# Kernel tuning notes

Hardware: AMD Instinct MI355X
Metric: run time of the kernel (lower is better)

Reference implementation:

```python
import jax, jax.numpy as jnp
import numpy as np

R = 512      # latent dim
M = 4        # center dimensionality
L = 256      # number of cluster centers
B = 8192     # batch
SIGMA_EPS = 1e-4


def setup_inputs() -> dict:
    key = jax.random.key(0)
    kx, kc = jax.random.split(key)
    x = jax.random.normal(kx, (B, R), dtype=jnp.float32)
    c = jax.random.normal(kc, (M, L), dtype=jnp.float32)   # codebook centers
    sigma = jnp.full((1,), 5.0, dtype=jnp.float32)         # trainable temperature
    return {"x": x, "c": c, "sigma": sigma}


def reference(x, c, sigma):
    b = x.shape[0]
    nf = R // M
    z = x.reshape(b, nf, M)                                # (b, nf, m)
    sig = jax.nn.relu(sigma[0]) + SIGMA_EPS
    # squared distances ||z - c||^2 over m, expanded to avoid (b,nf,m,L) materialization
    z_sq = jnp.sum(z * z, axis=-1, keepdims=True)          # (b, nf, 1)
    c_sq = jnp.sum(c * c, axis=0)                          # (L,)
    zc = jnp.einsum('bnm,ml->bnl', z, c)                   # (b, nf, L)
    dist = z_sq - 2.0 * zc + c_sq[None, None, :]           # (b, nf, L)
    q = jax.nn.softmax(-sig * dist, axis=-1)               # soft assignments (b, nf, L)
    out = jnp.einsum('bnl,ml->bnm', q, c)                  # weighted centers (b, nf, m)
    return out.reshape(b, R)
```

## Files before the change

### kernel.cpp

```cpp
#include <hip/hip_runtime.h>
#include <math.h>

#define RDIM 512
#define MDIM 4
#define LDIM 256
#define BDIM 8192
#define NROWS (BDIM * (RDIM / MDIM))
#define SIGMA_EPS 1e-4f
#define LOG2E 1.4426950408889634f

typedef _Float16 half4_t __attribute__((ext_vector_type(4)));
typedef _Float16 half8_t __attribute__((ext_vector_type(8)));
typedef __fp16   fp16x2_t __attribute__((ext_vector_type(2)));
typedef float    float4_t __attribute__((ext_vector_type(4)));

#define NRT (NROWS / 16)
#define MAIN_BLOCKS 2048
#define WPB 4
#define NT (NRT / (MAIN_BLOCKS * WPB))

__global__ void prep_kernel(const float* __restrict__ c, const float* __restrict__ sigma,
                            _Float16* __restrict__ a1w, _Float16* __restrict__ a2w) {
  const int gid  = blockIdx.x * 256 + threadIdx.x;
  const int lane = gid & 63;
  const int q4   = lane >> 4;
  const int m    = lane & 15;
  const float sig   = fmaxf(sigma[0], 0.0f) + SIGMA_EPS;
  const float sigL  = sig * LOG2E;
  const float sig2L = 2.0f * sigL;
  if (gid < 1024) {
    const int t = gid >> 6;
    const int l = t * 16 + m;
    float cv[4];
    cv[0] = c[l]; cv[1] = c[256 + l]; cv[2] = c[512 + l]; cv[3] = c[768 + l];
    _Float16 uh[4], ul[4];
    #pragma unroll
    for (int i = 0; i < 4; ++i) {
      float u = sig2L * cv[i];
      uh[i] = (_Float16)u;
      ul[i] = (_Float16)(u - (float)uh[i]);
    }
    float bias = -sigL * fmaf(cv[0], cv[0], fmaf(cv[1], cv[1], fmaf(cv[2], cv[2], cv[3] * cv[3])));
    _Float16 bh = (_Float16)bias;
    _Float16 bl = (_Float16)(bias - (float)bh);
    #pragma unroll
    for (int j = 0; j < 8; ++j) {
      int k = q4 * 8 + j;
      _Float16 v = (_Float16)0.0f;
      if      (k < 4)   v = uh[k];
      else if (k < 8)   v = uh[k - 4];
      else if (k < 12)  v = ul[k - 8];
      else if (k == 12) v = bh;
      else if (k == 13) v = bl;
      a1w[(t * 64 + lane) * 8 + j] = v;
    }
  } else if (gid < 1536) {
    const int p = (gid - 1024) >> 6;
    #pragma unroll
    for (int j = 0; j < 8; ++j) {
      int center = 32 * p + 16 * (j >> 2) + 4 * q4 + (j & 3);
      _Float16 v = (_Float16)0.0f;
      if (m < 4)       v = (_Float16)c[m * 256 + center];
      else if (m == 4) v = (_Float16)1.0f;
      a2w[(p * 64 + lane) * 8 + j] = v;
    }
  }
}

__global__ __launch_bounds__(256, 2) void sq_mfma_kernel(
    const float4* __restrict__ x4,
    const _Float16* __restrict__ a1w,
    const _Float16* __restrict__ a2w,
    float4* __restrict__ out4) {
  const int tid  = threadIdx.x;
  const int lane = tid & 63;
  const int wave = tid >> 6;
  const int q4   = lane >> 4;
  const int zr   = lane & 15;

  half8_t a1[16], a2[8];
  const half8_t* a1p = (const half8_t*)a1w;
  const half8_t* a2p = (const half8_t*)a2w;
  #pragma unroll
  for (int t = 0; t < 16; ++t) a1[t] = a1p[t * 64 + lane];
  #pragma unroll
  for (int p = 0; p < 8; ++p) a2[p] = a2p[p * 64 + lane];

  const int gw = blockIdx.x * WPB + wave;
  const float4_t zero4 = {0.f, 0.f, 0.f, 0.f};

  for (int it = 0; it < NT; ++it) {
    const int rowbase = (gw * NT + it) * 16;

    const float4 z = x4[rowbase + zr];
    _Float16 zh0 = (_Float16)z.x, zh1 = (_Float16)z.y, zh2 = (_Float16)z.z, zh3 = (_Float16)z.w;
    _Float16 zl0 = (_Float16)(z.x - (float)zh0);
    _Float16 zl1 = (_Float16)(z.y - (float)zh1);
    _Float16 zl2 = (_Float16)(z.z - (float)zh2);
    _Float16 zl3 = (_Float16)(z.w - (float)zh3);

    const _Float16 h0 = (_Float16)0.0f, h1 = (_Float16)1.0f;
    half8_t b1;
    b1[0] = (q4 < 2) ? zh0 : h0;
    b1[1] = (q4 < 2) ? zh1 : h0;
    b1[2] = (q4 < 2) ? zh2 : h0;
    b1[3] = (q4 < 2) ? zh3 : h0;
    b1[4] = (q4 == 0) ? zl0 : ((q4 == 1) ? h1 : h0);
    b1[5] = (q4 == 0) ? zl1 : ((q4 == 1) ? h1 : h0);
    b1[6] = (q4 == 0) ? zl2 : h0;
    b1[7] = (q4 == 0) ? zl3 : h0;

    float4_t s[16];
    #pragma unroll
    for (int t = 0; t < 16; ++t)
      s[t] = __builtin_amdgcn_mfma_f32_16x16x32_f16(a1[t], b1, zero4, 0, 0, 0);

    float mx = -3.0e38f;
    #pragma unroll
    for (int t = 0; t < 16; ++t)
      mx = fmaxf(mx, fmaxf(fmaxf(s[t][0], s[t][1]), fmaxf(s[t][2], s[t][3])));
    mx = fmaxf(mx, __shfl_xor(mx, 16));
    mx = fmaxf(mx, __shfl_xor(mx, 32));

    float4_t d2 = zero4;
    #pragma unroll
    for (int p = 0; p < 8; ++p) {
      fp16x2_t e01a = __builtin_amdgcn_cvt_pkrtz(
          __builtin_amdgcn_exp2f(s[2 * p][0] - mx), __builtin_amdgcn_exp2f(s[2 * p][1] - mx));
      fp16x2_t e23a = __builtin_amdgcn_cvt_pkrtz(
          __builtin_amdgcn_exp2f(s[2 * p][2] - mx), __builtin_amdgcn_exp2f(s[2 * p][3] - mx));
      fp16x2_t e01b = __builtin_amdgcn_cvt_pkrtz(
          __builtin_amdgcn_exp2f(s[2 * p + 1][0] - mx), __builtin_amdgcn_exp2f(s[2 * p + 1][1] - mx));
      fp16x2_t e23b = __builtin_amdgcn_cvt_pkrtz(
          __builtin_amdgcn_exp2f(s[2 * p + 1][2] - mx), __builtin_amdgcn_exp2f(s[2 * p + 1][3] - mx));
      half8_t b2;
      b2[0] = (_Float16)e01a[0]; b2[1] = (_Float16)e01a[1];
      b2[2] = (_Float16)e23a[0]; b2[3] = (_Float16)e23a[1];
      b2[4] = (_Float16)e01b[0]; b2[5] = (_Float16)e01b[1];
      b2[6] = (_Float16)e23b[0]; b2[7] = (_Float16)e23b[1];
      d2 = __builtin_amdgcn_mfma_f32_16x16x32_f16(a2[p], b2, d2, 0, 0, 0);
    }

    float den = __shfl(d2[0], zr + 16);
    if (lane < 16) {
      float r = __builtin_amdgcn_rcpf(den);
      float4 o = make_float4(d2[0] * r, d2[1] * r, d2[2] * r, d2[3] * r);
      out4[rowbase + zr] = o;
    }
  }
}

extern "C" void kernel_launch(void* const* d_in, const int* in_sizes, int n_in,
                              void* d_out, int out_size, void* d_ws, size_t ws_size,
                              hipStream_t stream) {
  const float4* x4    = (const float4*)d_in[0];
  const float*  c     = (const float*)d_in[1];
  const float*  sigma = (const float*)d_in[2];
  float4*       out4  = (float4*)d_out;

  _Float16* a1w = (_Float16*)d_ws;
  _Float16* a2w = a1w + 16 * 64 * 8;

  prep_kernel<<<6, 256, 0, stream>>>(c, sigma, a1w, a2w);
  sq_mfma_kernel<<<MAIN_BLOCKS, 256, 0, stream>>>(x4, a1w, a2w, out4);
}
```

Measured before the change: 120.1 us.

## Recompute logits with K=16 MFMA and fold max subtraction into matmul

The first-stage distance matmul moves from 16x16x32 to 16x16x16 MFMA with a compacted operand layout, shrinking the resident A1 fragments. The 16 logit tiles are no longer kept live across the max reduction. They are recomputed in the second pass, with the row max subtracted inside the MFMA through a hi/lo fp16 bias column, which removes the per-element subtraction. Launch bounds rise to 4 blocks per SM to use the lower register pressure for occupancy, at the cost of doubling the first-stage MFMA work and adding fp16 rounding error on the max term.

```diff
diff --git a/kernel.cpp b/kernel.cpp
--- a/kernel.cpp
+++ b/kernel.cpp
@@ -44,15 +44,12 @@
     _Float16 bh = (_Float16)bias;
     _Float16 bl = (_Float16)(bias - (float)bh);
     #pragma unroll
-    for (int j = 0; j < 8; ++j) {
-      int k = q4 * 8 + j;
-      _Float16 v = (_Float16)0.0f;
-      if      (k < 4)   v = uh[k];
-      else if (k < 8)   v = uh[k - 4];
-      else if (k < 12)  v = ul[k - 8];
-      else if (k == 12) v = bh;
-      else if (k == 13) v = bl;
-      a1w[(t * 64 + lane) * 8 + j] = v;
+    for (int j = 0; j < 4; ++j) {
+      _Float16 v;
+      if      (q4 <  2) v = uh[j];
+      else if (q4 == 2) v = ul[j];
+      else              v = (j == 0) ? bh : ((j == 1) ? bl : (_Float16)1.0f);
+      a1w[(t * 64 + lane) * 4 + j] = v;
     }
   } else if (gid < 1536) {
     const int p = (gid - 1024) >> 6;
@@ -67,7 +64,10 @@
   }
 }
 
-__global__ __launch_bounds__(256, 2) void sq_mfma_kernel(
+union U2H4 { uint2 u; half4_t h; };
+union H4X2 { fp16x2_t e[4]; half8_t h8; };
+
+__global__ __launch_bounds__(256, 4) void sq_mfma_kernel(
     const float4* __restrict__ x4,
     const _Float16* __restrict__ a1w,
     const _Float16* __restrict__ a2w,
@@ -78,8 +78,9 @@
   const int q4   = lane >> 4;
   const int zr   = lane & 15;
 
-  half8_t a1[16], a2[8];
-  const half8_t* a1p = (const half8_t*)a1w;
+  half4_t a1[16];
+  half8_t a2[8];
+  const half4_t* a1p = (const half4_t*)a1w;
   const half8_t* a2p = (const half8_t*)a2w;
   #pragma unroll
   for (int t = 0; t < 16; ++t) a1[t] = a1p[t * 64 + lane];
@@ -88,57 +89,50 @@
 
   const int gw = blockIdx.x * WPB + wave;
   const float4_t zero4 = {0.f, 0.f, 0.f, 0.f};
+  const unsigned one_one = 0x3C003C00u;
 
   for (int it = 0; it < NT; ++it) {
     const int rowbase = (gw * NT + it) * 16;
 
     const float4 z = x4[rowbase + zr];
-    _Float16 zh0 = (_Float16)z.x, zh1 = (_Float16)z.y, zh2 = (_Float16)z.z, zh3 = (_Float16)z.w;
-    _Float16 zl0 = (_Float16)(z.x - (float)zh0);
-    _Float16 zl1 = (_Float16)(z.y - (float)zh1);
-    _Float16 zl2 = (_Float16)(z.z - (float)zh2);
-    _Float16 zl3 = (_Float16)(z.w - (float)zh3);
+    fp16x2_t zh01 = __builtin_amdgcn_cvt_pkrtz(z.x, z.y);
+    fp16x2_t zh23 = __builtin_amdgcn_cvt_pkrtz(z.z, z.w);
+    fp16x2_t zl01 = __builtin_amdgcn_cvt_pkrtz(z.x - (float)zh01[0], z.y - (float)zh01[1]);
+    fp16x2_t zl23 = __builtin_amdgcn_cvt_pkrtz(z.z - (float)zh23[0], z.w - (float)zh23[1]);
+    const unsigned zh01u = __builtin_bit_cast(unsigned, zh01);
+    const unsigned zh23u = __builtin_bit_cast(unsigned, zh23);
+    const unsigned zl01u = __builtin_bit_cast(unsigned, zl01);
+    const unsigned zl23u = __builtin_bit_cast(unsigned, zl23);
 
-    const _Float16 h0 = (_Float16)0.0f, h1 = (_Float16)1.0f;
-    half8_t b1;
-    b1[0] = (q4 < 2) ? zh0 : h0;
-    b1[1] = (q4 < 2) ? zh1 : h0;
-    b1[2] = (q4 < 2) ? zh2 : h0;
-    b1[3] = (q4 < 2) ? zh3 : h0;
-    b1[4] = (q4 == 0) ? zl0 : ((q4 == 1) ? h1 : h0);
-    b1[5] = (q4 == 0) ? zl1 : ((q4 == 1) ? h1 : h0);
-    b1[6] = (q4 == 0) ? zl2 : h0;
-    b1[7] = (q4 == 0) ? zl3 : h0;
-
-    float4_t s[16];
-    #pragma unroll
-    for (int t = 0; t < 16; ++t)
-      s[t] = __builtin_amdgcn_mfma_f32_16x16x32_f16(a1[t], b1, zero4, 0, 0, 0);
+    const unsigned w0 = (q4 == 1) ? zl01u : ((q4 == 3) ? one_one : zh01u);
+    const unsigned w1A = (q4 == 3) ? 0u : ((q4 == 1) ? zl23u : zh23u);
+    U2H4 b1a; b1a.u = make_uint2(w0, w1A);
 
     float mx = -3.0e38f;
     #pragma unroll
-    for (int t = 0; t < 16; ++t)
-      mx = fmaxf(mx, fmaxf(fmaxf(s[t][0], s[t][1]), fmaxf(s[t][2], s[t][3])));
+    for (int t = 0; t < 16; ++t) {
+      float4_t s = __builtin_amdgcn_mfma_f32_16x16x16f16(a1[t], b1a.h, zero4, 0, 0, 0);
+      mx = fmaxf(fmaxf(mx, fmaxf(s[0], s[1])), fmaxf(s[2], s[3]));
+    }
     mx = fmaxf(mx, __shfl_xor(mx, 16));
     mx = fmaxf(mx, __shfl_xor(mx, 32));
+
+    float mhf = (float)(_Float16)mx;
+    fp16x2_t nm = __builtin_amdgcn_cvt_pkrtz(-mhf, -(mx - mhf));
+    const unsigned w1B = (q4 == 3) ? __builtin_bit_cast(unsigned, nm) : w1A;
+    U2H4 b1b; b1b.u = make_uint2(w0, w1B);
 
     float4_t d2 = zero4;
     #pragma unroll
     for (int p = 0; p < 8; ++p) {
-      fp16x2_t e01a = __builtin_amdgcn_cvt_pkrtz(
-          __builtin_amdgcn_exp2f(s[2 * p][0] - mx), __builtin_amdgcn_exp2f(s[2 * p][1] - mx));
-      fp16x2_t e23a = __builtin_amdgcn_cvt_pkrtz(
-          __builtin_amdgcn_exp2f(s[2 * p][2] - mx), __builtin_amdgcn_exp2f(s[2 * p][3] - mx));
-      fp16x2_t e01b = __builtin_amdgcn_cvt_pkrtz(
-          __builtin_amdgcn_exp2f(s[2 * p + 1][0] - mx), __builtin_amdgcn_exp2f(s[2 * p + 1][1] - mx));
-      fp16x2_t e23b = __builtin_amdgcn_cvt_pkrtz(
-          __builtin_amdgcn_exp2f(s[2 * p + 1][2] - mx), __builtin_amdgcn_exp2f(s[2 * p + 1][3] - mx));
-      half8_t b2;
-      b2[0] = (_Float16)e01a[0]; b2[1] = (_Float16)e01a[1];
-      b2[2] = (_Float16)e23a[0]; b2[3] = (_Float16)e23a[1];
-      b2[4] = (_Float16)e01b[0]; b2[5] = (_Float16)e01b[1];
-      b2[6] = (_Float16)e23b[0]; b2[7] = (_Float16)e23b[1];
-      d2 = __builtin_amdgcn_mfma_f32_16x16x32_f16(a2[p], b2, d2, 0, 0, 0);
+      float4_t sa = __builtin_amdgcn_mfma_f32_16x16x16f16(a1[2 * p],     b1b.h, zero4, 0, 0, 0);
+      float4_t sb = __builtin_amdgcn_mfma_f32_16x16x16f16(a1[2 * p + 1], b1b.h, zero4, 0, 0, 0);
+      H4X2 b2;
+      b2.e[0] = __builtin_amdgcn_cvt_pkrtz(__builtin_amdgcn_exp2f(sa[0]), __builtin_amdgcn_exp2f(sa[1]));
+      b2.e[1] = __builtin_amdgcn_cvt_pkrtz(__builtin_amdgcn_exp2f(sa[2]), __builtin_amdgcn_exp2f(sa[3]));
+      b2.e[2] = __builtin_amdgcn_cvt_pkrtz(__builtin_amdgcn_exp2f(sb[0]), __builtin_amdgcn_exp2f(sb[1]));
+      b2.e[3] = __builtin_amdgcn_cvt_pkrtz(__builtin_amdgcn_exp2f(sb[2]), __builtin_amdgcn_exp2f(sb[3]));
+      d2 = __builtin_amdgcn_mfma_f32_16x16x32_f16(a2[p], b2.h8, d2, 0, 0, 0);
     }
 
     float den = __shfl(d2[0], zr + 16);
@@ -159,7 +153,7 @@
   float4*       out4  = (float4*)d_out;
 
   _Float16* a1w = (_Float16*)d_ws;
-  _Float16* a2w = a1w + 16 * 64 * 8;
+  _Float16* a2w = a1w + 16 * 64 * 4;
 
   prep_kernel<<<6, 256, 0, stream>>>(c, sigma, a1w, a2w);
   sq_mfma_kernel<<<MAIN_BLOCKS, 256, 0, stream>>>(x4, a1w, a2w, out4);
```

After: 114.7 us. 1.05x faster.
